# Kernel tuning notes

Hardware: AMD Instinct MI355X
Metric: run time of the kernel (lower is better)

The kernel has to match this reference:

```python
import jax, jax.numpy as jnp
import numpy as np

H_DIM = 64
GRID = 8
NS = 2.0  # neighborhood_size


def _pool_seq(hidden, pos):
    # hidden: (P, H_DIM) hidden states of peds in one scene; pos: (P, 2) end positions
    P = hidden.shape[0]
    g2 = GRID * GRID
    tl_x = pos[:, 0] - NS / 2
    tl_y = pos[:, 1] + NS / 2
    br_x = pos[:, 0] + NS / 2
    br_y = pos[:, 1] - NS / 2
    # pair (i, j): grid of ped i (rows), position of ped j (cols)
    ox = pos[None, :, 0]
    oy = pos[None, :, 1]
    cell_x = jnp.floor((ox - tl_x[:, None]) / NS * GRID)
    cell_y = jnp.floor((tl_y[:, None] - oy) / NS * GRID)
    grid_pos = (cell_x + cell_y * GRID).astype(jnp.int32)
    # out-of-bound if outside neighborhood box OR i == j (diagonal forced out)
    oob = ((ox >= br_x[:, None]) | (ox <= tl_x[:, None])
           | (oy >= tl_y[:, None]) | (oy <= br_y[:, None])
           | jnp.eye(P, dtype=bool))
    idx = grid_pos + 1 + (jnp.arange(P, dtype=jnp.int32) * g2)[:, None]
    idx = jnp.where(oob, 0, idx)  # slot 0 is the trash bin (dropped below)
    src = jnp.broadcast_to(hidden[None], (P, P, H_DIM)).reshape(P * P, H_DIM)
    buf = jnp.zeros((P * g2 + 1, H_DIM), hidden.dtype)
    buf = buf.at[idx.reshape(-1)].add(src)
    return buf[1:].reshape(P, g2 * H_DIM)


def reference(h_states, seq_start_end, end_pos, rel_pos, W, b):
    B = end_pos.shape[0]
    S = seq_start_end.shape[0]
    P = B // S  # equal-length scenes -> static reshape
    hidden = h_states.reshape(-1, H_DIM).reshape(S, P, H_DIM)
    pos = end_pos.reshape(S, P, 2)
    pooled = jax.vmap(_pool_seq)(hidden, pos).reshape(B, GRID * GRID * H_DIM)
    # make_mlp([4096, 1024], relu, batch_norm=False): Linear -> ReLU
    return jax.nn.relu(pooled @ W + b)


def setup_inputs():
    key = jax.random.key(0)
    k0, k1, k2, k3 = jax.random.split(key, 4)
    S, P = 64, 64
    B = S * P
    bottleneck = 1024
    feat = GRID * GRID * H_DIM  # 4096
    h_states = jax.random.normal(k0, (1, B, H_DIM), jnp.float32)
    starts = jnp.arange(S, dtype=jnp.int32) * P
    seq_start_end = jnp.stack([starts, starts + P], axis=1)
    end_pos = jax.random.normal(k1, (B, 2), jnp.float32)
    rel_pos = jax.random.normal(k2, (B, 2), jnp.float32)
    W = jax.random.normal(k3, (feat, bottleneck), jnp.float32) * 0.02
    b = jnp.zeros((bottleneck,), jnp.float32)
    return {"h_states": h_states, "seq_start_end": seq_start_end,
            "end_pos": end_pos, "rel_pos": rel_pos, "W": W, "b": b}
```

## Files before the change

### kernel.cpp

```cpp
#include <hip/hip_runtime.h>


#define BM 128
#define BN 64
#define BK 128

typedef short short8 __attribute__((ext_vector_type(8)));
typedef short short4v __attribute__((ext_vector_type(4)));
typedef float floatx16 __attribute__((ext_vector_type(16)));

__device__ inline short f2bf(float x) {
    union { float f; unsigned u; } v; v.f = x;
    unsigned r = v.u + 0x7fffu + ((v.u >> 16) & 1u);
    return (short)(r >> 16);
}

__device__ inline void gload_lds16(const void* g, void* l) {
    __builtin_amdgcn_global_load_lds(
        (const __attribute__((address_space(1))) void*)g,
        (__attribute__((address_space(3))) void*)l,
        16, 0, 0);
}

__global__ __launch_bounds__(256) void prep_kernel(
    const float* __restrict__ h,
    const float* __restrict__ pos,
    short* __restrict__ pooled,
    const float* __restrict__ W,
    short* __restrict__ Wt,
    int K, int N, int poolBlocks)
{
    __shared__ __align__(16) unsigned char sh[18944];
    const int tid = threadIdx.x;

    if ((int)blockIdx.x < poolBlocks) {
        float* hs = (float*)sh;
        float* px = (float*)(sh + 16384);
        float* py = (float*)(sh + 16640);
        unsigned long long* wmask = (unsigned long long*)(sh + 16896);

        const int lane = tid & 63;
        const int w    = tid >> 6;
        const int s    = blockIdx.x >> 4;
        const int grp  = blockIdx.x & 15;
        const size_t base = (size_t)s * 64;

        const float4* hv  = (const float4*)(h + base * 64);
        float4*       hsv = (float4*)hs;
        #pragma unroll
        for (int c = 0; c < 4; ++c) hsv[tid + c * 256] = hv[tid + c * 256];
        if (tid < 64) {
            float2 p = ((const float2*)pos)[base + tid];
            px[tid] = p.x; py[tid] = p.y;
        }
        wmask[w * 64 + lane] = 0ull;
        __syncthreads();

        const int i = grp * 4 + w;
        const float tlx = px[i] - 1.0f;
        const float tly = py[i] + 1.0f;
        const float brx = px[i] + 1.0f;
        const float bry = py[i] - 1.0f;

        {
            const int j = lane;
            const float ox = px[j], oy = py[j];
            if (ox < brx && ox > tlx && oy < tly && oy > bry && j != i) {
                int cx = (int)floorf((ox - tlx) * 4.0f);
                int cy = (int)floorf((tly - oy) * 4.0f);
                atomicOr(&wmask[w * 64 + cx + cy * 8], 1ull << j);
            }
        }

        const int half = lane >> 5;
        const int d0   = (lane & 31) * 2;
        const size_t orow = (base + i) * 4096;
        unsigned short* pooledU = (unsigned short*)pooled;
        for (int c = 0; c < 64; c += 2) {
            unsigned long long m = wmask[w * 64 + c + half];
            float ax = 0.f, ay = 0.f;
            while (m) {
                int j0 = __builtin_ctzll(m); m &= m - 1;
                float2 hv2 = *(const float2*)&hs[j0 * 64 + d0];
                ax += hv2.x; ay += hv2.y;
            }
            unsigned pk = ((unsigned)(unsigned short)f2bf(ay) << 16)
                        |  (unsigned short)f2bf(ax);
            *(unsigned*)&pooledU[orow + (size_t)(c + half) * 64 + d0] = pk;
        }
    } else {
        float* t = (float*)sh;
        const int bid = blockIdx.x - poolBlocks;
        const int k0 = (bid & 63) * 64;
        const int n0 = (bid >> 6) * 64;

        const int r  = tid >> 4;
        const int cq = (tid & 15) * 4;
        #pragma unroll
        for (int i2 = 0; i2 < 4; ++i2) {
            const int row = r + i2 * 16;
            float4 v = *(const float4*)&W[(size_t)(k0 + row) * N + n0 + cq];
            t[row * 65 + cq + 0] = v.x; t[row * 65 + cq + 1] = v.y;
            t[row * 65 + cq + 2] = v.z; t[row * 65 + cq + 3] = v.w;
        }
        __syncthreads();
        const int nl = tid >> 4;
        const int kq = (tid & 15) * 4;
        #pragma unroll
        for (int i2 = 0; i2 < 4; ++i2) {
            const int n = nl + i2 * 16;
            short4v o;
            o.x = f2bf(t[(kq + 0) * 65 + n]); o.y = f2bf(t[(kq + 1) * 65 + n]);
            o.z = f2bf(t[(kq + 2) * 65 + n]); o.w = f2bf(t[(kq + 3) * 65 + n]);
            *(short4v*)&Wt[(size_t)(n0 + n) * K + k0 + kq] = o;
        }
    }
}

__global__ __launch_bounds__(256) void gemm_bias_relu(
    const short* __restrict__ A,
    const short* __restrict__ Bt,
    const float* __restrict__ bias,
    float* __restrict__ out,
    int M, int N, int K)
{
    __shared__ __align__(16) short As[BM * BK];
    __shared__ __align__(16) short Bs[BN * BK];

    const int tid  = threadIdx.x;
    const int lane = tid & 63;
    const int wave = tid >> 6;
    const int wr = wave >> 1;
    const int wc = wave & 1;
    const int nl = lane & 31;
    const int hl = lane >> 5;
    const int ml = lane & 15;

    const int b  = blockIdx.x;
    const int ib = b >> 3;
    const int m0 = ((b & 7) * 4 + (ib >> 4)) * BM;
    const int n0 = (ib & 15) * BN;

    const int r4   = lane >> 4;
    const int slot = lane & 15;

    const short* ag[8];
    const short* bg[4];
    #pragma unroll
    for (int c = 0; c < 8; ++c) {
        const int gi = c * 4 + wave;
        const int rl = gi * 4 + r4;
        ag[c] = A + (size_t)(m0 + rl) * K + (slot ^ (rl & 15)) * 8;
    }
    #pragma unroll
    for (int c = 0; c < 4; ++c) {
        const int gi = c * 4 + wave;
        const int rl = gi * 4 + r4;
        bg[c] = Bt + (size_t)(n0 + rl) * K + (slot ^ (rl & 15)) * 8;
    }

    floatx16 acc[2];
    #pragma unroll
    for (int mt = 0; mt < 2; ++mt)
        #pragma unroll
        for (int r = 0; r < 16; ++r) acc[mt][r] = 0.f;

    for (int kb = 0; kb < K; kb += BK) {
        if (kb) __syncthreads();
        #pragma unroll
        for (int c = 0; c < 8; ++c) {
            gload_lds16(ag[c], &As[(c * 4 + wave) * 512]);
            ag[c] += BK;
        }
        #pragma unroll
        for (int c = 0; c < 4; ++c) {
            gload_lds16(bg[c], &Bs[(c * 4 + wave) * 512]);
            bg[c] += BK;
        }
        __syncthreads();

        #pragma unroll
        for (int t = 0; t < 8; ++t) {
            const int g  = 2 * t + hl;
            short8 a0 = *(const short8*)&As[(wr * 64 +      nl) * BK + ((g ^ ml) * 8)];
            short8 a1 = *(const short8*)&As[(wr * 64 + 32 + nl) * BK + ((g ^ ml) * 8)];
            short8 bfr = *(const short8*)&Bs[(wc * 32 +     nl) * BK + ((g ^ ml) * 8)];
            acc[0] = __builtin_amdgcn_mfma_f32_32x32x16_bf16(a0, bfr, acc[0], 0, 0, 0);
            acc[1] = __builtin_amdgcn_mfma_f32_32x32x16_bf16(a1, bfr, acc[1], 0, 0, 0);
        }
    }

    const int gn = n0 + wc * 32 + nl;
    const float bv = bias[gn];
    #pragma unroll
    for (int mt = 0; mt < 2; ++mt) {
        #pragma unroll
        for (int r = 0; r < 16; ++r) {
            const int row32 = (r & 3) + 8 * (r >> 2) + 4 * hl;
            const int gm = m0 + wr * 64 + mt * 32 + row32;
            float v = acc[mt][r] + bv;
            out[(size_t)gm * N + gn] = v > 0.f ? v : 0.f;
        }
    }
}

extern "C" void kernel_launch(void* const* d_in, const int* in_sizes, int n_in,
                              void* d_out, int out_size, void* d_ws, size_t ws_size,
                              hipStream_t stream) {
    const float* h    = (const float*)d_in[0];
    const float* pos  = (const float*)d_in[2];
    const float* W    = (const float*)d_in[4];
    const float* bias = (const float*)d_in[5];

    const int B = in_sizes[0] / 64;
    const int N = in_sizes[5];
    const int K = 64 * 64;

    short* pooled = (short*)d_ws;
    short* Wt     = pooled + (size_t)B * K;
    float* out    = (float*)d_out;

    const int poolBlocks = B / 4;
    const int castBlocks = (K / 64) * (N / 64);
    prep_kernel<<<poolBlocks + castBlocks, 256, 0, stream>>>(
        h, pos, pooled, W, Wt, K, N, poolBlocks);
    gemm_bias_relu<<<(B / BM) * (N / BN), 256, 0, stream>>>(
        pooled, Wt, bias, out, B, N, K);
}
```

Before: 130.6 us.

## Split K across wave pairs in GEMM and reduce partial sums through LDS

Each wave now covers a 64x64 output tile over half of every BK slice, where before it covered a 64x32 tile over the full slice. Each A fragment is reused for two MFMAs and each B fragment for two, so the LDS reads per MFMA drop. The two wave halves then combine their partial accumulators through LDS before the bias and ReLU epilogue. This costs twice the accumulator registers, two extra barriers and an LDS reduction, and only half the waves write output.

```diff
diff --git a/kernel.cpp b/kernel.cpp
--- a/kernel.cpp
+++ b/kernel.cpp
@@ -131,7 +131,7 @@
     const int lane = tid & 63;
     const int wave = tid >> 6;
     const int wr = wave >> 1;
-    const int wc = wave & 1;
+    const int kh = wave & 1;
     const int nl = lane & 31;
     const int hl = lane >> 5;
     const int ml = lane & 15;
@@ -159,11 +159,11 @@
         bg[c] = Bt + (size_t)(n0 + rl) * K + (slot ^ (rl & 15)) * 8;
     }
 
-    floatx16 acc[2];
+    floatx16 acc[4];
     #pragma unroll
-    for (int mt = 0; mt < 2; ++mt)
-        #pragma unroll
-        for (int r = 0; r < 16; ++r) acc[mt][r] = 0.f;
+    for (int i = 0; i < 4; ++i)
+        #pragma unroll
+        for (int r = 0; r < 16; ++r) acc[i][r] = 0.f;
 
     for (int kb = 0; kb < K; kb += BK) {
         if (kb) __syncthreads();
@@ -180,27 +180,54 @@
         __syncthreads();
 
         #pragma unroll
-        for (int t = 0; t < 8; ++t) {
-            const int g  = 2 * t + hl;
-            short8 a0 = *(const short8*)&As[(wr * 64 +      nl) * BK + ((g ^ ml) * 8)];
-            short8 a1 = *(const short8*)&As[(wr * 64 + 32 + nl) * BK + ((g ^ ml) * 8)];
-            short8 bfr = *(const short8*)&Bs[(wc * 32 +     nl) * BK + ((g ^ ml) * 8)];
-            acc[0] = __builtin_amdgcn_mfma_f32_32x32x16_bf16(a0, bfr, acc[0], 0, 0, 0);
-            acc[1] = __builtin_amdgcn_mfma_f32_32x32x16_bf16(a1, bfr, acc[1], 0, 0, 0);
-        }
-    }
-
-    const int gn = n0 + wc * 32 + nl;
-    const float bv = bias[gn];
-    #pragma unroll
-    for (int mt = 0; mt < 2; ++mt) {
-        #pragma unroll
-        for (int r = 0; r < 16; ++r) {
-            const int row32 = (r & 3) + 8 * (r >> 2) + 4 * hl;
-            const int gm = m0 + wr * 64 + mt * 32 + row32;
-            float v = acc[mt][r] + bv;
-            out[(size_t)gm * N + gn] = v > 0.f ? v : 0.f;
-        }
+        for (int t = 0; t < 4; ++t) {
+            const int g  = kh * 8 + 2 * t + hl;
+            const int go = (g ^ ml) * 8;
+            short8 a0 = *(const short8*)&As[(wr * 64 +      nl) * BK + go];
+            short8 a1 = *(const short8*)&As[(wr * 64 + 32 + nl) * BK + go];
+            short8 b0 = *(const short8*)&Bs[(          nl) * BK + go];
+            short8 b1 = *(const short8*)&Bs[(     32 + nl) * BK + go];
+            acc[0] = __builtin_amdgcn_mfma_f32_32x32x16_bf16(a0, b0, acc[0], 0, 0, 0);
+            acc[1] = __builtin_amdgcn_mfma_f32_32x32x16_bf16(a0, b1, acc[1], 0, 0, 0);
+            acc[2] = __builtin_amdgcn_mfma_f32_32x32x16_bf16(a1, b0, acc[2], 0, 0, 0);
+            acc[3] = __builtin_amdgcn_mfma_f32_32x32x16_bf16(a1, b1, acc[3], 0, 0, 0);
+        }
+    }
+
+    __syncthreads();
+    float* red = (float*)As;
+    if (kh) {
+        #pragma unroll
+        for (int mi = 0; mi < 2; ++mi)
+            #pragma unroll
+            for (int ni = 0; ni < 2; ++ni)
+                #pragma unroll
+                for (int r = 0; r < 16; ++r) {
+                    const int row32 = (r & 3) + 8 * (r >> 2) + 4 * hl;
+                    red[wr * 4096 + (mi * 32 + row32) * 64 + ni * 32 + nl] =
+                        acc[mi * 2 + ni][r];
+                }
+    }
+    __syncthreads();
+    if (!kh) {
+        const float bv0 = bias[n0 + nl];
+        const float bv1 = bias[n0 + 32 + nl];
+        #pragma unroll
+        for (int mi = 0; mi < 2; ++mi)
+            #pragma unroll
+            for (int ni = 0; ni < 2; ++ni) {
+                const float bv = ni ? bv1 : bv0;
+                #pragma unroll
+                for (int r = 0; r < 16; ++r) {
+                    const int row32 = (r & 3) + 8 * (r >> 2) + 4 * hl;
+                    const int gm = m0 + wr * 64 + mi * 32 + row32;
+                    const int gn = n0 + ni * 32 + nl;
+                    float v = acc[mi * 2 + ni][r]
+                            + red[wr * 4096 + (mi * 32 + row32) * 64 + ni * 32 + nl]
+                            + bv;
+                    out[(size_t)gm * N + gn] = v > 0.f ? v : 0.f;
+                }
+            }
     }
 }
 
```

Result: no change. 131.4 us (+0.6%).

## Fuse pooling, weight cast and GEMM into one cooperative kernel with grid sync

Applied to the files above, without the earlier changes.

Merges the prep kernel and the GEMM kernel into a single cooperative launch of 512 blocks. Each block first does two pooling work units and then two weight-transpose/cast units, and a grid-wide barrier separates these from the GEMM phase. The aim is to remove the second kernel launch and the gap between the two kernels. In exchange it adds grid sync overhead and hardcodes the grid size to match the problem shape. Running all phases in one kernel may also limit occupancy.

```diff
diff --git a/kernel.cpp b/kernel.cpp
--- a/kernel.cpp
+++ b/kernel.cpp
@@ -1,4 +1,7 @@
 #include <hip/hip_runtime.h>
+#include <hip/hip_cooperative_groups.h>
+
+namespace cg = cooperative_groups;
 
 
 #define BM 128
@@ -8,6 +11,7 @@
 typedef short short8 __attribute__((ext_vector_type(8)));
 typedef short short4v __attribute__((ext_vector_type(4)));
 typedef float floatx16 __attribute__((ext_vector_type(16)));
+typedef unsigned long long u64;
 
 __device__ inline short f2bf(float x) {
     union { float f; unsigned u; } v; v.f = x;
@@ -22,27 +26,30 @@
         16, 0, 0);
 }
 
-__global__ __launch_bounds__(256) void prep_kernel(
+__global__ __launch_bounds__(256) void fused_all(
     const float* __restrict__ h,
     const float* __restrict__ pos,
+    const float* __restrict__ W,
+    const float* __restrict__ bias,
     short* __restrict__ pooled,
-    const float* __restrict__ W,
     short* __restrict__ Wt,
-    int K, int N, int poolBlocks)
+    float* __restrict__ out,
+    int M, int N, int K)
 {
-    __shared__ __align__(16) unsigned char sh[18944];
-    const int tid = threadIdx.x;
-
-    if ((int)blockIdx.x < poolBlocks) {
-        float* hs = (float*)sh;
-        float* px = (float*)(sh + 16384);
-        float* py = (float*)(sh + 16640);
-        unsigned long long* wmask = (unsigned long long*)(sh + 16896);
-
-        const int lane = tid & 63;
+    __shared__ __align__(16) unsigned char shbuf[49152];
+    const int tid  = threadIdx.x;
+    const int lane = tid & 63;
+
+    for (int u = 0; u < 2; ++u) {
+        const int p = (int)blockIdx.x * 2 + u;
+        float* hs = (float*)shbuf;
+        float* px = (float*)(shbuf + 16384);
+        float* py = (float*)(shbuf + 16640);
+        u64*   wmask = (u64*)(shbuf + 16896);
+
         const int w    = tid >> 6;
-        const int s    = blockIdx.x >> 4;
-        const int grp  = blockIdx.x & 15;
+        const int s    = p >> 4;
+        const int grp  = p & 15;
         const size_t base = (size_t)s * 64;
 
         const float4* hv  = (const float4*)(h + base * 64);
@@ -50,8 +57,8 @@
         #pragma unroll
         for (int c = 0; c < 4; ++c) hsv[tid + c * 256] = hv[tid + c * 256];
         if (tid < 64) {
-            float2 p = ((const float2*)pos)[base + tid];
-            px[tid] = p.x; py[tid] = p.y;
+            float2 pp = ((const float2*)pos)[base + tid];
+            px[tid] = pp.x; py[tid] = pp.y;
         }
         wmask[w * 64 + lane] = 0ull;
         __syncthreads();
@@ -77,7 +84,7 @@
         const size_t orow = (base + i) * 4096;
         unsigned short* pooledU = (unsigned short*)pooled;
         for (int c = 0; c < 64; c += 2) {
-            unsigned long long m = wmask[w * 64 + c + half];
+            u64 m = wmask[w * 64 + c + half];
             float ax = 0.f, ay = 0.f;
             while (m) {
                 int j0 = __builtin_ctzll(m); m &= m - 1;
@@ -88,47 +95,47 @@
                         |  (unsigned short)f2bf(ax);
             *(unsigned*)&pooledU[orow + (size_t)(c + half) * 64 + d0] = pk;
         }
-    } else {
-        float* t = (float*)sh;
-        const int bid = blockIdx.x - poolBlocks;
-        const int k0 = (bid & 63) * 64;
-        const int n0 = (bid >> 6) * 64;
+        __syncthreads();
+    }
+
+    for (int u = 0; u < 2; ++u) {
+        const int cb = (int)blockIdx.x * 2 + u;
+        float* t = (float*)shbuf;
+        const int k0 = (cb & 63) * 64;
+        const int n0c = (cb >> 6) * 64;
 
         const int r  = tid >> 4;
         const int cq = (tid & 15) * 4;
         #pragma unroll
         for (int i2 = 0; i2 < 4; ++i2) {
             const int row = r + i2 * 16;
-            float4 v = *(const float4*)&W[(size_t)(k0 + row) * N + n0 + cq];
+            float4 v = *(const float4*)&W[(size_t)(k0 + row) * N + n0c + cq];
             t[row * 65 + cq + 0] = v.x; t[row * 65 + cq + 1] = v.y;
             t[row * 65 + cq + 2] = v.z; t[row * 65 + cq + 3] = v.w;
         }
         __syncthreads();
-        const int nl = tid >> 4;
+        const int nl2 = tid >> 4;
         const int kq = (tid & 15) * 4;
         #pragma unroll
         for (int i2 = 0; i2 < 4; ++i2) {
-            const int n = nl + i2 * 16;
+            const int n = nl2 + i2 * 16;
             short4v o;
             o.x = f2bf(t[(kq + 0) * 65 + n]); o.y = f2bf(t[(kq + 1) * 65 + n]);
             o.z = f2bf(t[(kq + 2) * 65 + n]); o.w = f2bf(t[(kq + 3) * 65 + n]);
-            *(short4v*)&Wt[(size_t)(n0 + n) * K + k0 + kq] = o;
-        }
-    }
-}
-
-__global__ __launch_bounds__(256) void gemm_bias_relu(
-    const short* __restrict__ A,
-    const short* __restrict__ Bt,
-    const float* __restrict__ bias,
-    float* __restrict__ out,
-    int M, int N, int K)
-{
-    __shared__ __align__(16) short As[BM * BK];
-    __shared__ __align__(16) short Bs[BN * BK];
-
-    const int tid  = threadIdx.x;
-    const int lane = tid & 63;
+            *(short4v*)&Wt[(size_t)(n0c + n) * K + k0 + kq] = o;
+        }
+        __syncthreads();
+    }
+
+    __threadfence();
+    cg::this_grid().sync();
+    __threadfence();
+
+    const short* A  = pooled;
+    const short* Bt = Wt;
+    short* As  = (short*)shbuf;
+    short* Bsm = (short*)(shbuf + 32768);
+
     const int wave = tid >> 6;
     const int wr = wave >> 1;
     const int wc = wave & 1;
@@ -174,7 +181,7 @@
         }
         #pragma unroll
         for (int c = 0; c < 4; ++c) {
-            gload_lds16(bg[c], &Bs[(c * 4 + wave) * 512]);
+            gload_lds16(bg[c], &Bsm[(c * 4 + wave) * 512]);
             bg[c] += BK;
         }
         __syncthreads();
@@ -182,9 +189,9 @@
         #pragma unroll
         for (int t = 0; t < 8; ++t) {
             const int g  = 2 * t + hl;
-            short8 a0 = *(const short8*)&As[(wr * 64 +      nl) * BK + ((g ^ ml) * 8)];
-            short8 a1 = *(const short8*)&As[(wr * 64 + 32 + nl) * BK + ((g ^ ml) * 8)];
-            short8 bfr = *(const short8*)&Bs[(wc * 32 +     nl) * BK + ((g ^ ml) * 8)];
+            short8 a0  = *(const short8*)&As[(wr * 64 +      nl) * BK + ((g ^ ml) * 8)];
+            short8 a1  = *(const short8*)&As[(wr * 64 + 32 + nl) * BK + ((g ^ ml) * 8)];
+            short8 bfr = *(const short8*)&Bsm[(wc * 32 +     nl) * BK + ((g ^ ml) * 8)];
             acc[0] = __builtin_amdgcn_mfma_f32_32x32x16_bf16(a0, bfr, acc[0], 0, 0, 0);
             acc[1] = __builtin_amdgcn_mfma_f32_32x32x16_bf16(a1, bfr, acc[1], 0, 0, 0);
         }
@@ -212,18 +219,19 @@
     const float* W    = (const float*)d_in[4];
     const float* bias = (const float*)d_in[5];
 
-    const int B = in_sizes[0] / 64;
-    const int N = in_sizes[5];
-    const int K = 64 * 64;
+    int B = in_sizes[0] / 64;
+    int N = in_sizes[5];
+    int K = 64 * 64;
 
     short* pooled = (short*)d_ws;
     short* Wt     = pooled + (size_t)B * K;
     float* out    = (float*)d_out;
 
-    const int poolBlocks = B / 4;
-    const int castBlocks = (K / 64) * (N / 64);
-    prep_kernel<<<poolBlocks + castBlocks, 256, 0, stream>>>(
-        h, pos, pooled, W, Wt, K, N, poolBlocks);
-    gemm_bias_relu<<<(B / BM) * (N / BN), 256, 0, stream>>>(
-        pooled, Wt, bias, out, B, N, K);
-}
+    void* args[] = {
+        (void*)&h, (void*)&pos, (void*)&W, (void*)&bias,
+        (void*)&pooled, (void*)&Wt, (void*)&out,
+        (void*)&B, (void*)&N, (void*)&K
+    };
+    hipLaunchCooperativeKernel(reinterpret_cast<void*>(&fused_all),
+                               dim3(512), dim3(256), args, 0, stream);
+}
```

Result: slower. 297.6 us (+127.8%).
